# Performance work log

Hardware: AMD Instinct MI355X
Metric: run time of the kernel (lower is better)

The kernel has to match this reference:

```python
import jax, jax.numpy as jnp
import numpy as np

H = 32
DECAY = 0.9


def setup_inputs() -> dict:
    key = jax.random.key(0)
    ks = jax.random.split(key, 6)
    B, T, D = 8, 4096, 1024
    x = jax.random.normal(ks[0], (B, T, D), dtype=jnp.float32)
    s = 1.0 / np.sqrt(D)
    Wv = jax.random.normal(ks[1], (D, D), dtype=jnp.float32) * s
    bv = jax.random.normal(ks[2], (D,), dtype=jnp.float32) * s
    Wo = jax.random.normal(ks[3], (D, D), dtype=jnp.float32) * s
    bo = jax.random.normal(ks[4], (D,), dtype=jnp.float32) * s
    w = jnp.asarray(DECAY ** np.arange(H), dtype=jnp.float32)
    decay_w = w / jnp.sum(w)
    return {"x": x, "Wv": Wv, "bv": bv, "Wo": Wo, "bo": bo, "decay_w": decay_w}


def reference(x, Wv, bv, Wo, bo, decay_w):
    # x: [B, T, D]. Original pads H zeros at front and unfolds windows of size H
    # with stride 1, producing T+1 windows: window t covers x[t-H .. t-1].
    # value_proj is linear and applied to every window copy, so it commutes with
    # the fixed-weight sum: attended = (sum_i w_i * x_window_i) @ Wv^T + bv*sum(w).
    B, T, D = x.shape
    Hlen = decay_w.shape[0]
    x_pad = jnp.pad(x, ((0, 0), (Hlen, 0), (0, 0)))  # [B, T+H, D]
    # Depthwise 1D conv over time with the (shared) decay kernel.
    kernel = jnp.broadcast_to(decay_w[:, None, None], (Hlen, 1, D))  # [W, I=1, O=D]
    s = jax.lax.conv_general_dilated(
        x_pad, kernel, window_strides=(1,), padding="VALID",
        dimension_numbers=("NWC", "WIO", "NWC"), feature_group_count=D,
    )  # [B, T+1, D]
    attended = s @ Wv.T + bv * jnp.sum(decay_w)
    return attended @ Wo.T + bo  # [B, T+1, D]
```

## Files before the change

kernel.cpp:

```cpp
#include <hip/hip_runtime.h>
#include <stdint.h>

#define D_DIM 1024
#define T_DIM 4096
#define B_DIM 8
#define M_REAL (B_DIM * (T_DIM + 1))
#define M_MAIN 32768
#define NWG 512

typedef short short8 __attribute__((ext_vector_type(8)));
typedef float floatx4 __attribute__((ext_vector_type(4)));

typedef const __attribute__((address_space(1))) void* gptr_t;
typedef __attribute__((address_space(3))) void* lptr_t;

__device__ __forceinline__ ushort f2bf(float f) {
  union { float f; uint32_t u; } v; v.f = f;
  uint32_t r = v.u + 0x7FFF + ((v.u >> 16) & 1);
  return (ushort)(r >> 16);
}
__device__ __forceinline__ float bf2f(ushort b) {
  union { uint32_t u; float f; } v; v.u = ((uint32_t)b) << 16; return v.f;
}

#define BARRIER()  asm volatile("s_barrier" ::: "memory")
#define WAIT_VM2() asm volatile("s_waitcnt vmcnt(2)" ::: "memory")
#define WAIT_VM0() asm volatile("s_waitcnt vmcnt(0)" ::: "memory")
#define WAIT_LGKM0() do { asm volatile("s_waitcnt lgkmcnt(0)" ::: "memory"); \
                          __builtin_amdgcn_sched_barrier(0); } while (0)
#define SP1() __builtin_amdgcn_s_setprio(1)
#define SP0() __builtin_amdgcn_s_setprio(0)

__global__ __launch_bounds__(1024) void gemm_w16_kernel(
    const ushort* __restrict__ A, const ushort* __restrict__ Bm,
    float* __restrict__ C, const float* __restrict__ bias)
{
  __shared__ char smem[98304];
  const int tid  = threadIdx.x;
  const int wave = tid >> 6;
  const int lane = tid & 63;
  const int wm = wave >> 2, wn = wave & 3;
  const int l15 = lane & 15, lhi = lane >> 4;

  const int bid = blockIdx.x;
  const int wg  = (bid & 7) * 64 + (bid >> 3);
  const int n0 = (wg & 3) * 256;
  const int m0 = (wg >> 2) * 256;

  const int srow = tid >> 2;
  const int ksw  = ((tid & 3) ^ ((tid >> 3) & 3)) * 8;
  const ushort* Aq = A  + (size_t)(m0 + srow) * D_DIM + ksw;
  const ushort* Bq = Bm + (size_t)(n0 + srow) * D_DIM + ksw;

  const int xorc = (lhi ^ ((l15 >> 1) & 3)) * 16;
  const int aoff = (wm * 64 + l15) * 64 + xorc;
  const int boff = (wn * 64 + l15) * 64 + xorc;

  short8 a[4], b[4];
  floatx4 acc[4][4] = {};

#define STAGE_W(S) do { \
  __builtin_amdgcn_global_load_lds((gptr_t)(Aq + koff), \
      (lptr_t)(smem + (S) * 16384 + wave * 1024), 16, 0, 0); \
  __builtin_amdgcn_global_load_lds((gptr_t)(Bq + koff), \
      (lptr_t)(smem + 49152 + (S) * 16384 + wave * 1024), 16, 0, 0); \
  koff += 32; \
} while (0)

#define LDAB_W(S) do { \
  _Pragma("unroll") \
  for (int m = 0; m < 4; ++m) \
    a[m] = *(const short8*)(smem + (S) * 16384 + aoff + m * 1024); \
  _Pragma("unroll") \
  for (int n = 0; n < 4; ++n) \
    b[n] = *(const short8*)(smem + 49152 + (S) * 16384 + boff + n * 1024); \
} while (0)

#define MFMA_W() do { \
  _Pragma("unroll") \
  for (int m = 0; m < 4; ++m) \
    _Pragma("unroll") \
    for (int n = 0; n < 4; ++n) \
      acc[m][n] = __builtin_amdgcn_mfma_f32_16x16x32_bf16( \
          a[m], b[n], acc[m][n], 0, 0, 0); \
} while (0)

#define ITER_W(S0, S2, STG, VMW) do { \
  VMW; \
  BARRIER(); \
  if (STG) STAGE_W(S2); \
  LDAB_W(S0); \
  WAIT_LGKM0(); \
  SP1(); MFMA_W(); SP0(); \
} while (0)

  int koff = 0;
  STAGE_W(0);
  STAGE_W(1);

#pragma unroll 1
  for (int it = 0; it < 10; ++it) {
    ITER_W(0, 2, 1, WAIT_VM2());
    ITER_W(1, 0, 1, WAIT_VM2());
    ITER_W(2, 1, 1, WAIT_VM2());
  }
  ITER_W(0, 2, 0, WAIT_VM2());
  ITER_W(1, 0, 0, WAIT_VM0());

#pragma unroll
  for (int m = 0; m < 4; ++m)
#pragma unroll
    for (int n = 0; n < 4; ++n) {
      const int gn = n0 + wn * 64 + n * 16 + l15;
      const float bia = bias[gn];
#pragma unroll
      for (int j = 0; j < 4; ++j) {
        const int gm = m0 + wm * 64 + m * 16 + lhi * 4 + j;
        C[(size_t)gm * D_DIM + gn] = acc[m][n][j] + bia;
      }
    }
#undef STAGE_W
#undef LDAB_W
#undef MFMA_W
#undef ITER_W
}

__global__ __launch_bounds__(256) void tail_gemv_kernel(
    const ushort* __restrict__ S, const ushort* __restrict__ Wf,
    const float* __restrict__ cvec, float* __restrict__ out)
{
  const int wavei = threadIdx.x >> 6, lane = threadIdx.x & 63;
  const int c = blockIdx.x * 4 + wavei;
  float acc[8] = {};
  for (int i = 0; i < 16; ++i) {
    const int k = i * 64 + lane;
    const float wv = bf2f(Wf[(size_t)c * D_DIM + k]);
#pragma unroll
    for (int r = 0; r < 8; ++r)
      acc[r] += wv * bf2f(S[(size_t)(M_MAIN + r) * D_DIM + k]);
  }
#pragma unroll
  for (int r = 0; r < 8; ++r) {
#pragma unroll
    for (int off = 32; off; off >>= 1) acc[r] += __shfl_xor(acc[r], off, 64);
  }
  if (lane == 0) {
    const float bia = cvec[c];
#pragma unroll
    for (int r = 0; r < 8; ++r)
      out[(size_t)(M_MAIN + r) * D_DIM + c] = acc[r] + bia;
  }
}

__global__ __launch_bounds__(256) void gemm_bt_kernel(
    const ushort* __restrict__ A, const ushort* __restrict__ Bm,
    ushort* __restrict__ Cb, int K, int N)
{
  __shared__ ushort As[128][64];
  __shared__ ushort Bs[128][64];
  const int tid  = threadIdx.x;
  const int wave = tid >> 6;
  const int lane = tid & 63;
  const int wm = wave >> 1, wn = wave & 1;
  const int n0 = blockIdx.x * 128, m0 = blockIdx.y * 128;
  const int l15 = lane & 15, lhi = lane >> 4;

  floatx4 acc[4][4] = {};

  const int srow = tid >> 3;
  const int sk8  = (tid & 7) * 8;
  const ushort* Ab = A  + (size_t)(m0 + srow) * K + sk8;
  const ushort* Bb = Bm + (size_t)(n0 + srow) * K + sk8;

  for (int k0 = 0; k0 < K; k0 += 64) {
#pragma unroll
    for (int q = 0; q < 4; ++q)
      __builtin_amdgcn_global_load_lds((gptr_t)(Ab + k0 + (size_t)q * 32 * K),
          (lptr_t)((char*)&As[0][0] + (q * 256 + wave * 64) * 16), 16, 0, 0);
#pragma unroll
    for (int q = 0; q < 4; ++q)
      __builtin_amdgcn_global_load_lds((gptr_t)(Bb + k0 + (size_t)q * 32 * K),
          (lptr_t)((char*)&Bs[0][0] + (q * 256 + wave * 64) * 16), 16, 0, 0);
    __syncthreads();

#pragma unroll
    for (int kk = 0; kk < 2; ++kk) {
      short8 af[4], bfrg[4];
#pragma unroll
      for (int i = 0; i < 4; ++i) {
        af[i]   = *(const short8*)(&As[wm * 64 + i * 16 + l15][kk * 32 + lhi * 8]);
        bfrg[i] = *(const short8*)(&Bs[wn * 64 + i * 16 + l15][kk * 32 + lhi * 8]);
      }
#pragma unroll
      for (int mi = 0; mi < 4; ++mi)
#pragma unroll
        for (int ni = 0; ni < 4; ++ni)
          acc[mi][ni] = __builtin_amdgcn_mfma_f32_16x16x32_bf16(
              af[mi], bfrg[ni], acc[mi][ni], 0, 0, 0);
    }
    __syncthreads();
  }

#pragma unroll
  for (int mi = 0; mi < 4; ++mi)
#pragma unroll
    for (int ni = 0; ni < 4; ++ni) {
      const int gn = n0 + wn * 64 + ni * 16 + l15;
#pragma unroll
      for (int j = 0; j < 4; ++j) {
        const int gm = m0 + wm * 64 + mi * 16 + lhi * 4 + j;
        Cb[(size_t)gm * N + gn] = f2bf(acc[mi][ni][j]);
      }
    }
}

#define CTCH 256
__global__ __launch_bounds__(256) void conv_kernel(
    const float* __restrict__ x, const float* __restrict__ dw,
    ushort* __restrict__ S)
{
  const int b   = blockIdx.y;
  const int col = blockIdx.z * 256 + threadIdx.x;
  const int t0  = blockIdx.x * CTCH;

  float w[32];
#pragma unroll
  for (int i = 0; i < 32; ++i) w[i] = dw[i];
  const float rinv = w[0] / w[1];
  const float w31  = w[31];
  const float c0   = -w[0] * rinv;

  const float* xb = x + (size_t)b * T_DIM * D_DIM + col;
  ushort*      Sb = S + (size_t)b * (T_DIM + 1) * D_DIM + col;

  float prev[32], cur[32];
  float s;
  if (blockIdx.x == 0) {
#pragma unroll
    for (int i = 0; i < 32; ++i) prev[i] = 0.f;
    s = 0.f;
    Sb[0] = f2bf(0.f);
  } else {
#pragma unroll
    for (int i = 0; i < 32; ++i) prev[i] = xb[(size_t)(t0 - 32 + i) * D_DIM];
    s = 0.f;
#pragma unroll
    for (int i = 0; i < 32; ++i) s = __builtin_fmaf(w[i], prev[i], s);
  }

#pragma unroll 1
  for (int g = 0; g < 8; g += 2) {
#pragma unroll
    for (int i = 0; i < 32; ++i) cur[i] = xb[(size_t)(t0 + g * 32 + i) * D_DIM];
#pragma unroll
    for (int j = 0; j < 32; ++j) {
      s = __builtin_fmaf(s, rinv, __builtin_fmaf(prev[j], c0, w31 * cur[j]));
      Sb[(size_t)(t0 + g * 32 + 1 + j) * D_DIM] = f2bf(s);
    }
    s = 0.f;
#pragma unroll
    for (int i = 0; i < 32; ++i) s = __builtin_fmaf(w[i], cur[i], s);
#pragma unroll
    for (int i = 0; i < 32; ++i) prev[i] = xb[(size_t)(t0 + (g + 1) * 32 + i) * D_DIM];
#pragma unroll
    for (int j = 0; j < 32; ++j) {
      s = __builtin_fmaf(s, rinv, __builtin_fmaf(cur[j], c0, w31 * prev[j]));
      Sb[(size_t)(t0 + (g + 1) * 32 + 1 + j) * D_DIM] = f2bf(s);
    }
    s = 0.f;
#pragma unroll
    for (int i = 0; i < 32; ++i) s = __builtin_fmaf(w[i], prev[i], s);
  }
}

__global__ __launch_bounds__(256) void prep_kernel(
    const float* __restrict__ Wo, const float* __restrict__ Wv,
    const float* __restrict__ bv, const float* __restrict__ bo,
    const float* __restrict__ dw,
    ushort* __restrict__ WoB, ushort* __restrict__ WvT,
    float* __restrict__ cvec)
{
  __shared__ float tile[32][33];
  const int bid = blockIdx.x;
  const int tid = threadIdx.x;

  if (bid < 1024) {
    const int i = bid * 256 + tid;
    const float4 v = ((const float4*)Wo)[i];
    ushort4 o = make_ushort4(f2bf(v.x), f2bf(v.y), f2bf(v.z), f2bf(v.w));
    *(ushort4*)(WoB + (size_t)i * 4) = o;
  } else if (bid < 2048) {
    const int b2 = bid - 1024;
    const int c0 = (b2 & 31) * 32, r0 = (b2 >> 5) * 32;
    const int tx = tid & 31, ty = tid >> 5;
#pragma unroll
    for (int j = 0; j < 4; ++j)
      tile[ty + j * 8][tx] = Wv[(size_t)(r0 + ty + j * 8) * D_DIM + c0 + tx];
    __syncthreads();
#pragma unroll
    for (int j = 0; j < 4; ++j)
      WvT[(size_t)(c0 + ty + j * 8) * D_DIM + r0 + tx] = f2bf(tile[tx][ty + j * 8]);
  } else {
    const int j    = (bid - 2048) * 4 + (tid >> 6);
    const int lane = tid & 63;
    float sumw = 0.f;
#pragma unroll
    for (int i = 0; i < 32; ++i) sumw += dw[i];
    float s = 0.f;
    for (int k = lane; k < D_DIM; k += 64) s += Wo[(size_t)j * D_DIM + k] * bv[k];
#pragma unroll
    for (int off = 32; off; off >>= 1) s += __shfl_xor(s, off, 64);
    if (lane == 0) cvec[j] = sumw * s + bo[j];
  }
}

extern "C" void kernel_launch(void* const* d_in, const int* in_sizes, int n_in,
                              void* d_out, int out_size, void* d_ws, size_t ws_size,
                              hipStream_t stream) {
  const float* x  = (const float*)d_in[0];
  const float* Wv = (const float*)d_in[1];
  const float* bv = (const float*)d_in[2];
  const float* Wo = (const float*)d_in[3];
  const float* bo = (const float*)d_in[4];
  const float* dw = (const float*)d_in[5];
  float* out = (float*)d_out;

  char* ws = (char*)d_ws;
  ushort* S      = (ushort*)ws;
  ushort* WoB    = (ushort*)(ws + (size_t)M_REAL * D_DIM * 2);
  ushort* WvT    = WoB + (size_t)D_DIM * D_DIM;
  ushort* Wfused = WvT + (size_t)D_DIM * D_DIM;
  float*  cvec   = (float*)(Wfused + (size_t)D_DIM * D_DIM);

  prep_kernel<<<dim3(2304), dim3(256), 0, stream>>>(
      Wo, Wv, bv, bo, dw, WoB, WvT, cvec);

  gemm_bt_kernel<<<dim3(8, 8), dim3(256), 0, stream>>>(
      WoB, WvT, Wfused, D_DIM, D_DIM);

  conv_kernel<<<dim3(T_DIM / CTCH, B_DIM, 4), dim3(256), 0, stream>>>(x, dw, S);

  gemm_w16_kernel<<<dim3(NWG), dim3(1024), 0, stream>>>(S, Wfused, out, cvec);

  tail_gemv_kernel<<<dim3(256), dim3(256), 0, stream>>>(S, Wfused, cvec, out);
}
```

Baseline: 154.1 us.

## Switch GEMM to BK=64 double-buffered LDS pipeline with 8-way XOR swizzle

```diff
diff --git a/kernel.cpp b/kernel.cpp
--- a/kernel.cpp
+++ b/kernel.cpp
@@ -24,7 +24,6 @@
 }
 
 #define BARRIER()  asm volatile("s_barrier" ::: "memory")
-#define WAIT_VM2() asm volatile("s_waitcnt vmcnt(2)" ::: "memory")
 #define WAIT_VM0() asm volatile("s_waitcnt vmcnt(0)" ::: "memory")
 #define WAIT_LGKM0() do { asm volatile("s_waitcnt lgkmcnt(0)" ::: "memory"); \
                           __builtin_amdgcn_sched_barrier(0); } while (0)
@@ -35,45 +34,54 @@
     const ushort* __restrict__ A, const ushort* __restrict__ Bm,
     float* __restrict__ C, const float* __restrict__ bias)
 {
-  __shared__ char smem[98304];
+  __shared__ char smem[131072];
   const int tid  = threadIdx.x;
   const int wave = tid >> 6;
   const int lane = tid & 63;
   const int wm = wave >> 2, wn = wave & 3;
   const int l15 = lane & 15, lhi = lane >> 4;
+  const int rsw = (l15 & 7) << 4;
 
   const int bid = blockIdx.x;
   const int wg  = (bid & 7) * 64 + (bid >> 3);
   const int n0 = (wg & 3) * 256;
   const int m0 = (wg >> 2) * 256;
 
-  const int srow = tid >> 2;
-  const int ksw  = ((tid & 3) ^ ((tid >> 3) & 3)) * 8;
-  const ushort* Aq = A  + (size_t)(m0 + srow) * D_DIM + ksw;
-  const ushort* Bq = Bm + (size_t)(n0 + srow) * D_DIM + ksw;
-
-  const int xorc = (lhi ^ ((l15 >> 1) & 3)) * 16;
-  const int aoff = (wm * 64 + l15) * 64 + xorc;
-  const int boff = (wn * 64 + l15) * 64 + xorc;
+  const int srow = tid >> 3;
+  const int ksw  = ((tid & 7) ^ (srow & 7)) * 8;
+  const ushort* Aq0 = A  + (size_t)(m0 + srow) * D_DIM + ksw;
+  const ushort* Aq1 = A  + (size_t)(m0 + 128 + srow) * D_DIM + ksw;
+  const ushort* Bq0 = Bm + (size_t)(n0 + srow) * D_DIM + ksw;
+  const ushort* Bq1 = Bm + (size_t)(n0 + 128 + srow) * D_DIM + ksw;
 
   short8 a[4], b[4];
   floatx4 acc[4][4] = {};
 
 #define STAGE_W(S) do { \
-  __builtin_amdgcn_global_load_lds((gptr_t)(Aq + koff), \
-      (lptr_t)(smem + (S) * 16384 + wave * 1024), 16, 0, 0); \
-  __builtin_amdgcn_global_load_lds((gptr_t)(Bq + koff), \
-      (lptr_t)(smem + 49152 + (S) * 16384 + wave * 1024), 16, 0, 0); \
-  koff += 32; \
+  __builtin_amdgcn_global_load_lds((gptr_t)(Aq0 + koff), \
+      (lptr_t)(smem + (S) * 32768 + wave * 1024), 16, 0, 0); \
+  __builtin_amdgcn_global_load_lds((gptr_t)(Aq1 + koff), \
+      (lptr_t)(smem + (S) * 32768 + 16384 + wave * 1024), 16, 0, 0); \
+  __builtin_amdgcn_global_load_lds((gptr_t)(Bq0 + koff), \
+      (lptr_t)(smem + 65536 + (S) * 32768 + wave * 1024), 16, 0, 0); \
+  __builtin_amdgcn_global_load_lds((gptr_t)(Bq1 + koff), \
+      (lptr_t)(smem + 65536 + (S) * 32768 + 16384 + wave * 1024), 16, 0, 0); \
+  koff += 64; \
 } while (0)
 
-#define LDAB_W(S) do { \
+#define LDAB_W(S, KK) do { \
+  const char* _ab = smem + (S) * 32768; \
+  const char* _bb = smem + 65536 + (S) * 32768; \
   _Pragma("unroll") \
-  for (int m = 0; m < 4; ++m) \
-    a[m] = *(const short8*)(smem + (S) * 16384 + aoff + m * 1024); \
+  for (int m = 0; m < 4; ++m) { \
+    const int o = (((wm * 64 + m * 16 + l15) * 128 + (KK) * 64 + lhi * 16)) ^ rsw; \
+    a[m] = *(const short8*)(_ab + o); \
+  } \
   _Pragma("unroll") \
-  for (int n = 0; n < 4; ++n) \
-    b[n] = *(const short8*)(smem + 49152 + (S) * 16384 + boff + n * 1024); \
+  for (int n = 0; n < 4; ++n) { \
+    const int o = (((wn * 64 + n * 16 + l15) * 128 + (KK) * 64 + lhi * 16)) ^ rsw; \
+    b[n] = *(const short8*)(_bb + o); \
+  } \
 } while (0)
 
 #define MFMA_W() do { \
@@ -85,27 +93,28 @@
           a[m], b[n], acc[m][n], 0, 0, 0); \
 } while (0)
 
-#define ITER_W(S0, S2, STG, VMW) do { \
-  VMW; \
+#define ITER_W(S0, STG) do { \
+  WAIT_VM0(); \
   BARRIER(); \
-  if (STG) STAGE_W(S2); \
-  LDAB_W(S0); \
+  if (STG) STAGE_W((S0) ^ 1); \
+  LDAB_W(S0, 0); \
+  WAIT_LGKM0(); \
+  SP1(); MFMA_W(); SP0(); \
+  LDAB_W(S0, 1); \
   WAIT_LGKM0(); \
   SP1(); MFMA_W(); SP0(); \
 } while (0)
 
   int koff = 0;
   STAGE_W(0);
-  STAGE_W(1);
 
 #pragma unroll 1
-  for (int it = 0; it < 10; ++it) {
-    ITER_W(0, 2, 1, WAIT_VM2());
-    ITER_W(1, 0, 1, WAIT_VM2());
-    ITER_W(2, 1, 1, WAIT_VM2());
-  }
-  ITER_W(0, 2, 0, WAIT_VM2());
-  ITER_W(1, 0, 0, WAIT_VM0());
+  for (int it = 0; it < 7; ++it) {
+    ITER_W(0, 1);
+    ITER_W(1, 1);
+  }
+  ITER_W(0, 1);
+  ITER_W(1, 0);
 
 #pragma unroll
   for (int m = 0; m < 4; ++m)
```

New measurement: 157.0 us. About the same (+1.9%).
